# Optimization experiments

Measured on AMD Instinct MI355X. Metric: run time of the kernel, lower is better.

## Reference

```python
import jax, jax.numpy as jnp
import numpy as np

B, S, H, J, LAT, OBS = 256, 128, 1024, 12, 64, 51
NL = 13                  # fk_model link count
PD = (NL + 1) * 3        # pos_dim = 42
FPS = 30.0
ACT_SCALE = 0.25
SMIN, SMAX = 0.05, 0.5
PIN = 2 * J + OBS + LAT  # 139


def setup_inputs() -> dict:
    key = jax.random.key(0)
    ks = jax.random.split(key, 16)
    rn = lambda k, shape, s=0.02: jax.random.normal(k, shape, dtype=jnp.float32) * s
    return dict(
        z=jax.random.normal(ks[0], (B, LAT), jnp.float32),
        obs_seq=jax.random.normal(ks[1], (B, S, OBS), jnp.float32),
        W1=rn(ks[2], (H, PIN)), b1=jnp.zeros((H,), jnp.float32),
        g1=jnp.ones((H,), jnp.float32), be1=jnp.zeros((H,), jnp.float32),
        W2=rn(ks[3], (H, H)), b2=jnp.zeros((H,), jnp.float32),
        g2=jnp.ones((H,), jnp.float32), be2=jnp.zeros((H,), jnp.float32),
        Wa1=rn(ks[4], (H, H)), ba1=jnp.zeros((H,), jnp.float32),
        Wa2=rn(ks[5], (J, H)), ba2=jnp.zeros((J,), jnp.float32),
        Wo=rn(ks[6], (3, H)), bo=jnp.zeros((3,), jnp.float32),
        Wv=rn(ks[7], (PD, H)), bv=jnp.full((PD,), -2.0, jnp.float32),  # torch init: zeros weight, bias=-2 (we keep small random W for non-degenerate grads)
        alpha_logits=jnp.full((J,), float(np.log(0.3)), jnp.float32),
        fk_W=rn(ks[8], (NL * 3, J), 0.1), fk_b=rn(ks[9], (NL * 3,), 0.1),  # linear FK surrogate
        pos_mean=rn(ks[10], (NL + 1, 3), 0.1),
        pos_std=1.0 + jax.random.uniform(ks[11], (NL + 1, 3), jnp.float32),
        joint_lower=jnp.full((J,), -2.0, jnp.float32),
        joint_upper=jnp.full((J,), 2.0, jnp.float32),
        default_dof_pos=rn(ks[12], (J,), 0.3),
    )


def _layernorm(x, g, b):
    m = jnp.mean(x, axis=-1, keepdims=True)
    v = jnp.var(x, axis=-1, keepdims=True)
    return (x - m) * jax.lax.rsqrt(v + 1e-5) * g + b


def reference(z, obs_seq, W1, b1, g1, be1, W2, b2, g2, be2, Wa1, ba1, Wa2, ba2,
              Wo, bo, Wv, bv, alpha_logits, fk_W, fk_b, pos_mean, pos_std,
              joint_lower, joint_upper, default_dof_pos):
    j_range = (joint_upper - joint_lower) / 2.0
    j_mean = (joint_upper + joint_lower) / 2.0
    alpha = jax.nn.sigmoid(alpha_logits)
    Bsz = z.shape[0]

    def step(carry, obs_t):
        pj, pdq = carry                                 # [B,J] each
        jn = (pj - j_mean) / j_range
        x = jnp.concatenate([jn, pdq, obs_t, z], axis=-1)   # [B,PIN]
        h = jax.nn.relu(_layernorm(x @ W1.T + b1, g1, be1))
        h = jax.nn.relu(_layernorm(h @ W2.T + b2, g2, be2))  # [B,H]
        a = jnp.tanh(jax.nn.relu(h @ Wa1.T + ba1) @ Wa2.T + ba2)  # [B,J]
        tgt = a * ACT_SCALE + default_dof_pos
        cj = jnp.clip(pj + alpha * (tgt - pj), joint_lower, joint_upper)
        obj = h @ Wo.T + bo                             # [B,3]
        # torch detaches the carried state (prev_joints/prev_dq)
        cdq = (cj - pj) * FPS
        new_carry = (jax.lax.stop_gradient(cj), jax.lax.stop_gradient(cdq))
        return new_carry, (h, a, cj, obj)

    pj0 = jnp.broadcast_to(default_dof_pos, (Bsz, J))
    pdq0 = jnp.zeros((Bsz, J), z.dtype)
    _, (hs, acts, joints, objs) = jax.lax.scan(step, (pj0, pdq0), jnp.swapaxes(obs_seq, 0, 1))

    features_seq = jnp.swapaxes(hs, 0, 1)    # [B,S,H]
    actions_seq = jnp.swapaxes(acts, 0, 1)   # [B,S,J]
    joint_traj = jnp.swapaxes(joints, 0, 1)  # [B,S,J]
    object_traj = jnp.swapaxes(objs, 0, 1)   # [B,S,3]

    agent_traj = joint_traj @ fk_W.T + fk_b  # [B,S,NL*3] linear FK surrogate
    combined = jnp.concatenate([agent_traj, object_traj], axis=-1)
    combined = combined.reshape(Bsz, S, NL + 1, 3)
    graph_x_mu = ((combined - pos_mean) / pos_std).reshape(Bsz, S, -1)  # [B,S,PD]

    sigma = SMIN + (SMAX - SMIN) * jax.nn.sigmoid(features_seq @ Wv.T + bv)
    log_sigma_pos = jnp.log(sigma)           # [B,S,PD]
    return (graph_x_mu, joint_traj, actions_seq, log_sigma_pos)
```

## Files before the change

### kernel.cpp

```cpp
#include <hip/hip_runtime.h>
#include <math.h>


#define NB 256
#define NS 128
#define NH 1024
#define NJ 12
#define NPIN 139
#define NPD 42
#define WPG 32
#define BROW 32
#define W2S 1032
#define AS 1032
#define XJS 40
#define SLOTSTRIDE 1024

typedef __attribute__((ext_vector_type(8))) short short8;
typedef __attribute__((ext_vector_type(4))) float f32x4;
typedef __attribute__((ext_vector_type(4))) unsigned short u16x4;

struct Params {
  const float* z; const float* obs; const float* W1; const float* b1;
  const float* g1; const float* be1; const float* W2; const float* b2;
  const float* g2; const float* be2; const float* Wa1; const float* ba1;
  const float* Wa2; const float* ba2; const float* Wo; const float* bo;
  const float* Wv; const float* bv; const float* alog; const float* fkW;
  const float* fkb; const float* pmean; const float* pstd; const float* jlo;
  const float* jhi; const float* ddp;
  float* out_gmu; float* out_joint; float* out_act; float* out_ls;
  float* zc; float* pa; float* part2;
  unsigned short* y1b; unsigned short* y2b;
  unsigned short* wa1b; unsigned short* wexb; unsigned short* w1ab;
  unsigned int* gcnt; unsigned int* slots;
};

__device__ __forceinline__ unsigned short f2bf(float x) {
  union { float f; unsigned u; } v; v.f = x;
  unsigned r = v.u + 0x7FFFu + ((v.u >> 16) & 1u);
  return (unsigned short)(r >> 16);
}
__device__ __forceinline__ float bf2f(unsigned short x) {
  union { unsigned u; float f; } v; v.u = ((unsigned)x) << 16;
  return v.f;
}
__device__ __forceinline__ unsigned cvt_pk_bf16(float lo, float hi) {
  unsigned r;
  asm("v_cvt_pk_bf16_f32 %0, %1, %2" : "=v"(r) : "v"(lo), "v"(hi));
  return r;
}
__device__ __forceinline__ void ld16_sc0(const unsigned short* p, short8& d) {
  asm volatile("global_load_dwordx4 %0, %1, off sc0" : "=v"(d) : "v"(p));
}
__device__ __forceinline__ void ldf4_sc0(const float* p, f32x4& d) {
  asm volatile("global_load_dwordx4 %0, %1, off sc0" : "=v"(d) : "v"(p));
}
__device__ __forceinline__ void vwait0() {
  asm volatile("s_waitcnt vmcnt(0)" ::: "memory");
  __builtin_amdgcn_sched_barrier(0);
}

__device__ __forceinline__ f32x4 dot1024(const unsigned short* a, const unsigned short* b) {
  const short8* ap = (const short8*)a;
  const short8* bp = (const short8*)b;
  f32x4 acc0 = {0.f, 0.f, 0.f, 0.f};
  f32x4 acc1 = {0.f, 0.f, 0.f, 0.f};
#pragma unroll 4
  for (int k8 = 0; k8 < 128; k8 += 8) {
    acc0 = __builtin_amdgcn_mfma_f32_16x16x32_bf16(ap[k8], bp[k8], acc0, 0, 0, 0);
    acc1 = __builtin_amdgcn_mfma_f32_16x16x32_bf16(ap[k8 + 4], bp[k8 + 4], acc1, 0, 0, 0);
  }
  return acc0 + acc1;
}

__device__ __forceinline__ void gbar(unsigned int* c, unsigned int target) {
  __threadfence();
  __syncthreads();
  if (threadIdx.x == 0) {
    __hip_atomic_fetch_add(c, 1u, __ATOMIC_RELEASE, __HIP_MEMORY_SCOPE_AGENT);
    unsigned long long t0 = __builtin_amdgcn_s_memrealtime();
    while (__hip_atomic_load(c, __ATOMIC_ACQUIRE, __HIP_MEMORY_SCOPE_AGENT) < target) {
      __builtin_amdgcn_s_sleep(16);
      if (__builtin_amdgcn_s_memrealtime() - t0 > (1ull << 25)) break;
    }
  }
  __syncthreads();
  __threadfence();
}

__device__ __forceinline__ void slot_wait(const unsigned int* sg, unsigned target, int lane) {
  const unsigned int* myslot = sg + (size_t)(lane & 31) * SLOTSTRIDE;
  unsigned long long t0 = __builtin_amdgcn_s_memrealtime();
  for (;;) {
    unsigned v;
    asm volatile("global_load_dword %0, %1, off sc0 sc1\n\t"
                 "s_waitcnt vmcnt(0)"
                 : "=v"(v) : "v"(myslot) : "memory");
    if (__all(v >= target)) break;
    __builtin_amdgcn_s_sleep(1);
    if (__builtin_amdgcn_s_memrealtime() - t0 > (1ull << 23)) break;
  }
}
__device__ __forceinline__ void xbar2(unsigned int* sg, int w, unsigned target,
                                      int wave, int lane) {
  asm volatile("s_waitcnt vmcnt(0)" ::: "memory");
  __syncthreads();
  if (wave == 0) {
    if (lane == 0)
      __hip_atomic_fetch_add(sg + (size_t)w * SLOTSTRIDE, 1u, __ATOMIC_RELAXED,
                             __HIP_MEMORY_SCOPE_AGENT);
    slot_wait(sg, target, lane);
  }
  __syncthreads();
}

__global__ __launch_bounds__(256, 1) void decoder_persistent(Params p) {
  __shared__ unsigned short w2l[BROW * W2S];
  __shared__ unsigned short albuf[BROW * AS];
  __shared__ float g1l[NH], be1l[NH], g2l[NH], be2l[NH];
  __shared__ unsigned short t1l[BROW * 40];
  __shared__ unsigned short wa2l[16 * 40];
  __shared__ unsigned short xjl[BROW * XJS];
  __shared__ float pj_l[BROW * NJ], pdq_l[BROW * NJ];
  __shared__ float alpha_l[NJ], jm_l[NJ], jri_l[NJ], lo_l[NJ], hi_l[NJ], ddp_l[NJ], ba2_l[NJ];
  __shared__ float pm_l[NPD], psi_l[NPD], bv_l[NPD], bo_l[4];

  const int tid = threadIdx.x;
  const int bid = blockIdx.x;
  const int g = bid & 7;
  const int w = bid >> 3;
  const int b0 = g * BROW;
  const int n0 = w * 32;
  const int wave = tid >> 6;
  const int lane = tid & 63;

  unsigned int* sg = p.slots + (size_t)g * WPG * SLOTSTRIDE;
  unsigned short* y1bg = p.y1b + (size_t)g * BROW * NH;
  unsigned short* y2bg = p.y2b + (size_t)g * BROW * NH;
  float* pa_gg = p.pa + (size_t)g * BROW * NJ * 32;
  float* part2g = p.part2 + (size_t)g * BROW * 128;

  if (tid < NJ) {
    alpha_l[tid] = 1.f / (1.f + expf(-p.alog[tid]));
    float lo = p.jlo[tid], hi = p.jhi[tid];
    jm_l[tid] = 0.5f * (hi + lo);
    jri_l[tid] = 2.f / (hi - lo);
    lo_l[tid] = lo; hi_l[tid] = hi;
    ddp_l[tid] = p.ddp[tid]; ba2_l[tid] = p.ba2[tid];
  }
  if (tid < NPD) { pm_l[tid] = p.pmean[tid]; psi_l[tid] = 1.f / p.pstd[tid]; bv_l[tid] = p.bv[tid]; }
  if (tid < 3) bo_l[tid] = p.bo[tid];
  for (int idx = tid; idx < BROW * NJ; idx += 256) { pj_l[idx] = p.ddp[idx % NJ]; pdq_l[idx] = 0.f; }
  for (int idx = tid; idx < NH; idx += 256) {
    g1l[idx] = p.g1[idx]; be1l[idx] = p.be1[idx];
    g2l[idx] = p.g2[idx]; be2l[idx] = p.be2[idx];
  }
  for (int idx = tid; idx < BROW * NH; idx += 256) {
    int r = idx >> 10, k = idx & (NH - 1);
    w2l[r * W2S + k] = f2bf(p.W2[(size_t)(n0 + r) * NH + k]);
  }
  for (int idx = tid; idx < 16 * 32; idx += 256) {
    int rr = idx >> 5, cc = idx & 31;
    wa2l[rr * 40 + cc] = (rr < NJ) ? f2bf(p.Wa2[(size_t)rr * NH + n0 + cc]) : (unsigned short)0;
  }
  __syncthreads();
  for (int idx = tid; idx < BROW * 32; idx += 256) {
    int r = idx >> 5, k = idx & 31;
    float v = 0.f;
    if (k < NJ) v = (pj_l[r * NJ + k] - jm_l[k]) * jri_l[k];
    else if (k < 24) v = pdq_l[r * NJ + (k - 12)];
    xjl[r * XJS + k] = f2bf(v);
  }
  {
    int r = tid >> 3, cq = tid & 7;
    int nb = n0 + cq * 4;
    const float* zr = p.z + (size_t)(b0 + r) * 64;
    const float* w1z = p.W1 + (size_t)nb * NPIN + 75;
    float a0 = p.b1[nb], a1 = p.b1[nb + 1], a2 = p.b1[nb + 2], a3 = p.b1[nb + 3];
    for (int k = 0; k < 64; ++k) {
      float zv = zr[k];
      a0 += zv * w1z[k]; a1 += zv * w1z[NPIN + k];
      a2 += zv * w1z[2 * NPIN + k]; a3 += zv * w1z[3 * NPIN + k];
    }
    f32x4 st = {a0, a1, a2, a3};
    *(f32x4*)(p.zc + (size_t)(b0 + r) * NH + nb) = st;
    const float* w1r = p.W1 + (size_t)nb * NPIN;
    const float* ob = p.obs + (size_t)(b0 + r) * NS * 51;
    for (int o = 0; o < 51; ++o) {
      float ov = ob[o];
      st[0] += ov * w1r[24 + o]; st[1] += ov * w1r[NPIN + 24 + o];
      st[2] += ov * w1r[2 * NPIN + 24 + o]; st[3] += ov * w1r[3 * NPIN + 24 + o];
    }
    u16x4 hv = {f2bf(st[0]), f2bf(st[1]), f2bf(st[2]), f2bf(st[3])};
    *(u16x4*)(y1bg + (size_t)r * NH + nb) = hv;
  }
  for (int idx = tid; idx < 4 * NH; idx += 256) {
    int r = idx >> 10, k = idx & (NH - 1);
    int row = n0 + g * 4 + r;
    p.wa1b[(size_t)row * NH + k] = f2bf(p.Wa1[(size_t)row * NH + k]);
  }
  if (tid < 128) {
    int c2 = tid >> 5, k = tid & 31;
    int col = n0 + g * 4 + c2;
    p.w1ab[(size_t)col * 32 + k] =
        (k < 24) ? f2bf(p.W1[(size_t)col * NPIN + k]) : (unsigned short)0;
  }
  if (bid == 1) {
    for (int idx = tid; idx < 48 * NH; idx += 256) {
      int r = idx >> 10, k = idx & (NH - 1);
      unsigned short v = 0;
      if (r < 3) v = f2bf(p.Wo[(size_t)r * NH + k]);
      else if (r < 45) v = f2bf(p.Wv[(size_t)(r - 3) * NH + k]);
      p.wexb[idx] = v;
    }
  }
  gbar(p.gcnt, 256u);

  auto Ycorr = [&]() {
    const int kq = (lane >> 4) * 8;
    const int r0 = (lane >> 4) * 4;
    short8 a0 = *(const short8*)&xjl[(lane & 15) * XJS + kq];
    short8 a1 = *(const short8*)&xjl[(16 + (lane & 15)) * XJS + kq];
#pragma unroll
    for (int nt = 0; nt < 16; ++nt) {
      int col = (wave * 16 + nt) * 16 + (lane & 15);
      short8 b8 = *(const short8*)(p.w1ab + (size_t)col * 32 + kq);
      f32x4 z4 = {0.f, 0.f, 0.f, 0.f};
      f32x4 d0 = __builtin_amdgcn_mfma_f32_16x16x32_bf16(a0, b8, z4, 0, 0, 0);
      f32x4 d1 = __builtin_amdgcn_mfma_f32_16x16x32_bf16(a1, b8, z4, 0, 0, 0);
#pragma unroll
      for (int i = 0; i < 4; ++i) {
        albuf[(r0 + i) * AS + col] = f2bf(d0[i]);
        albuf[(16 + r0 + i) * AS + col] = f2bf(d1[i]);
      }
    }
  };

  auto Ystage = [&]() {
    const int r = tid >> 3, cq = tid & 7;
    const unsigned short* src = y1bg + (size_t)r * NH + cq * 8;
    unsigned short* dst = &albuf[r * AS + cq * 8];
    short8 vp[16];
#pragma unroll
    for (int i = 0; i < 16; ++i) ld16_sc0(src + (size_t)i * 64, vp[i]);
    vwait0();
    float s = 0.f, q = 0.f;
#pragma unroll
    for (int i = 0; i < 16; ++i) {
      short8 vc = *(const short8*)(dst + i * 64);
      short8 vs;
#pragma unroll
      for (int jj = 0; jj < 8; ++jj) {
        float x = bf2f((unsigned short)vp[i][jj]) + bf2f((unsigned short)vc[jj]);
        s += x; q = fmaf(x, x, q);
        vs[jj] = (short)f2bf(x);
      }
      vp[i] = vs;
    }
#pragma unroll
    for (int off = 4; off; off >>= 1) {
      s += __shfl_down(s, off, 8);
      q += __shfl_down(q, off, 8);
    }
    s = __shfl(s, 0, 8); q = __shfl(q, 0, 8);
    float m = s * (1.f / 1024.f);
    float rs = rsqrtf(q * (1.f / 1024.f) - m * m + 1e-5f);
    float nmrs = -m * rs;
#pragma unroll
    for (int i = 0; i < 16; ++i) {
      int c = cq * 8 + i * 64;
      f32x4 ga = *(const f32x4*)(g1l + c);
      f32x4 gb = *(const f32x4*)(g1l + c + 4);
      f32x4 ba = *(const f32x4*)(be1l + c);
      f32x4 bb = *(const f32x4*)(be1l + c + 4);
      float xn[8];
#pragma unroll
      for (int jj = 0; jj < 8; ++jj) {
        float x = bf2f((unsigned short)vp[i][jj]);
        float tn = fmaf(x, rs, nmrs);
        float gg = (jj < 4) ? ga[jj] : gb[jj - 4];
        float bv2 = (jj < 4) ? ba[jj] : bb[jj - 4];
        xn[jj] = fmaxf(fmaf(tn, gg, bv2), 0.f);
      }
      uint4 pk = {cvt_pk_bf16(xn[0], xn[1]), cvt_pk_bf16(xn[2], xn[3]),
                  cvt_pk_bf16(xn[4], xn[5]), cvt_pk_bf16(xn[6], xn[7])};
      *(uint4*)(dst + i * 64) = pk;
    }
  };

  auto Yphase = [&]() {
    Ycorr();
    __syncthreads();
    Ystage();
    __syncthreads();
    int rt = wave >> 1, ct = wave & 1;
    int kq = (lane >> 4) * 8;
    const unsigned short* a = &albuf[(rt * 16 + (lane & 15)) * AS + kq];
    const unsigned short* b = &w2l[(ct * 16 + (lane & 15)) * W2S + kq];
    f32x4 acc = dot1024(a, b);
    int col = n0 + ct * 16 + (lane & 15);
    float b2v = p.b2[col];
    float sv[4], qv[4];
#pragma unroll
    for (int i = 0; i < 4; ++i) {
      int row = rt * 16 + (lane >> 4) * 4 + i;
      float val = acc[i] + b2v;
      y2bg[(size_t)row * NH + col] = f2bf(val);
      sv[i] = val; qv[i] = val * val;
    }
#pragma unroll
    for (int mask = 1; mask < 16; mask <<= 1) {
#pragma unroll
      for (int i = 0; i < 4; ++i) {
        sv[i] += __shfl_xor(sv[i], mask, 64);
        qv[i] += __shfl_xor(qv[i], mask, 64);
      }
    }
    if ((lane & 15) == 0) {
      int rbase = rt * 16 + (lane >> 4) * 4;
#pragma unroll
      for (int i = 0; i < 4; ++i) {
        float* pw = part2g + (size_t)(rbase + i) * 128 + (w * 2 + ct) * 2;
        pw[0] = sv[i]; pw[1] = qv[i];
      }
    }
  };

  auto Zstage = [&]() {
    const int r = tid >> 3, cq = tid & 7;
    const unsigned short* src = y2bg + (size_t)r * NH + cq * 8;
    unsigned short* dst = &albuf[r * AS + cq * 8];
    short8 v[16];
#pragma unroll
    for (int i = 0; i < 16; ++i) ld16_sc0(src + (size_t)i * 64, v[i]);
    const float* pp = part2g + (size_t)r * 128 + cq * 16;
    f32x4 p0, p1, p2, p3;
    ldf4_sc0(pp, p0); ldf4_sc0(pp + 4, p1);
    ldf4_sc0(pp + 8, p2); ldf4_sc0(pp + 12, p3);
    vwait0();
    float s = p0[0] + p0[2] + p1[0] + p1[2] + p2[0] + p2[2] + p3[0] + p3[2];
    float q = p0[1] + p0[3] + p1[1] + p1[3] + p2[1] + p2[3] + p3[1] + p3[3];
#pragma unroll
    for (int off = 4; off; off >>= 1) {
      s += __shfl_down(s, off, 8);
      q += __shfl_down(q, off, 8);
    }
    s = __shfl(s, 0, 8); q = __shfl(q, 0, 8);
    float m = s * (1.f / 1024.f);
    float rs = rsqrtf(q * (1.f / 1024.f) - m * m + 1e-5f);
    float nmrs = -m * rs;
#pragma unroll
    for (int i = 0; i < 16; ++i) {
      int c = cq * 8 + i * 64;
      f32x4 ga = *(const f32x4*)(g2l + c);
      f32x4 gb = *(const f32x4*)(g2l + c + 4);
      f32x4 ba = *(const f32x4*)(be2l + c);
      f32x4 bb = *(const f32x4*)(be2l + c + 4);
      float xn[8];
#pragma unroll
      for (int jj = 0; jj < 8; ++jj) {
        float x = bf2f((unsigned short)v[i][jj]);
        float tn = fmaf(x, rs, nmrs);
        float gg = (jj < 4) ? ga[jj] : gb[jj - 4];
        float bv2 = (jj < 4) ? ba[jj] : bb[jj - 4];
        xn[jj] = fmaxf(fmaf(tn, gg, bv2), 0.f);
      }
      uint4 pk = {cvt_pk_bf16(xn[0], xn[1]), cvt_pk_bf16(xn[2], xn[3]),
                  cvt_pk_bf16(xn[4], xn[5]), cvt_pk_bf16(xn[6], xn[7])};
      *(uint4*)(dst + i * 64) = pk;
    }
  };

  auto Zphase = [&](int t) {
    Zstage();
    __syncthreads();
    int rt = wave >> 1, ct = wave & 1;
    int kq = (lane >> 4) * 8;
    {
      const unsigned short* a = &albuf[(rt * 16 + (lane & 15)) * AS + kq];
      const unsigned short* b = p.wa1b + (size_t)(n0 + ct * 16 + (lane & 15)) * NH + kq;
      f32x4 acc = dot1024(a, b);
      int lcol = ct * 16 + (lane & 15);
      float bav = p.ba1[n0 + lcol];
#pragma unroll
      for (int i = 0; i < 4; ++i) {
        int row = rt * 16 + (lane >> 4) * 4 + i;
        t1l[row * 40 + lcol] = f2bf(fmaxf(acc[i] + bav, 0.f));
      }
    }
    __syncthreads();
    if (wave < 2) {
      int k0 = (lane >> 4) * 8;
      short8 a8 = *(const short8*)&t1l[(wave * 16 + (lane & 15)) * 40 + k0];
      short8 b8 = *(const short8*)&wa2l[(lane & 15) * 40 + k0];
      f32x4 z4 = {0.f, 0.f, 0.f, 0.f};
      f32x4 d = __builtin_amdgcn_mfma_f32_16x16x32_bf16(a8, b8, z4, 0, 0, 0);
      int j = lane & 15;
      if (j < NJ) {
#pragma unroll
        for (int i = 0; i < 4; ++i) {
          int row = wave * 16 + (lane >> 4) * 4 + i;
          pa_gg[((size_t)row * NJ + j) * 32 + w] = d[i];
        }
      }
    }
    if (w >= 26 && wave == 3) {
      int e = w - 26, cte = e >> 1, rte = e & 1;
      const unsigned short* a = &albuf[(rte * 16 + (lane & 15)) * AS + kq];
      const unsigned short* b = p.wexb + (size_t)(cte * 16 + (lane & 15)) * NH + kq;
      f32x4 acc = dot1024(a, b);
      int ec = cte * 16 + (lane & 15);
#pragma unroll
      for (int i = 0; i < 4; ++i) {
        int row = rte * 16 + (lane >> 4) * 4 + i;
        int bb = b0 + row;
        if (ec < 3) {
          float val = acc[i] + bo_l[ec];
          p.out_gmu[((size_t)bb * NS + t) * NPD + 39 + ec] = (val - pm_l[39 + ec]) * psi_l[39 + ec];
        } else if (ec < 45) {
          int sv2 = ec - 3;
          float val = acc[i] + bv_l[sv2];
          float sig = 0.05f + 0.45f / (1.f + expf(-val));
          p.out_ls[((size_t)bb * NS + t) * NPD + sv2] = logf(sig);
        }
      }
    }
    if (t + 1 < NS) {
      int r = tid >> 3, cq = tid & 7;
      int nb = n0 + cq * 4;
      f32x4 acc = *(const f32x4*)(p.zc + (size_t)(b0 + r) * NH + nb);
      const float* w1r = p.W1 + (size_t)nb * NPIN;
      const float* ob = p.obs + ((size_t)(b0 + r) * NS + (t + 1)) * 51;
      for (int o = 0; o < 51; ++o) {
        float ov = ob[o];
        acc[0] += ov * w1r[24 + o]; acc[1] += ov * w1r[NPIN + 24 + o];
        acc[2] += ov * w1r[2 * NPIN + 24 + o]; acc[3] += ov * w1r[3 * NPIN + 24 + o];
      }
      u16x4 hv = {f2bf(acc[0]), f2bf(acc[1]), f2bf(acc[2]), f2bf(acc[3])};
      *(u16x4*)(y1bg + (size_t)r * NH + nb) = hv;
    }
  };

  auto Xmid = [&](int tp) {
    for (int e = tid; e < BROW * NJ; e += 256) {
      const float* pp = pa_gg + (size_t)e * 32;
      f32x4 u[8];
#pragma unroll
      for (int c2 = 0; c2 < 8; ++c2) ldf4_sc0(pp + c2 * 4, u[c2]);
      vwait0();
      f32x4 ss = ((u[0] + u[1]) + (u[2] + u[3])) + ((u[4] + u[5]) + (u[6] + u[7]));
      float sum = ss[0] + ss[1] + ss[2] + ss[3];
      int r = e / NJ, j = e - r * NJ;
      float av = tanhf(sum + ba2_l[j]);
      float pj = pj_l[e];
      float tgt = av * 0.25f + ddp_l[j];
      float cj = pj + alpha_l[j] * (tgt - pj);
      cj = fminf(fmaxf(cj, lo_l[j]), hi_l[j]);
      pdq_l[e] = (cj - pj) * 30.f;
      pj_l[e] = cj;
      if (w == 0) {
        size_t o = ((size_t)(b0 + r) * NS + tp) * NJ + j;
        p.out_joint[o] = cj;
        p.out_act[o] = av;
      }
    }
    __syncthreads();
    if (w == 0) {
      for (int idx = tid; idx < BROW * 39; idx += 256) {
        int r = idx / 39, m = idx - r * 39;
        float s = p.fkb[m];
        const float* fw = p.fkW + m * NJ;
#pragma unroll
        for (int j = 0; j < NJ; ++j) s += pj_l[r * NJ + j] * fw[j];
        p.out_gmu[((size_t)(b0 + r) * NS + tp) * NPD + m] = (s - pm_l[m]) * psi_l[m];
      }
    }
    for (int idx = tid; idx < BROW * 32; idx += 256) {
      int r = idx >> 5, k = idx & 31;
      float v = 0.f;
      if (k < NJ) v = (pj_l[r * NJ + k] - jm_l[k]) * jri_l[k];
      else if (k < 24) v = pdq_l[r * NJ + (k - 12)];
      xjl[r * XJS + k] = f2bf(v);
    }
    __syncthreads();
  };

  unsigned nbar = 0;
  for (int t = 0; t < NS; ++t) {
    Yphase();
    xbar2(sg, w, ++nbar, wave, lane);
    Zphase(t);
    xbar2(sg, w, ++nbar, wave, lane);
    Xmid(t);
  }
}

extern "C" void kernel_launch(void* const* d_in, const int* in_sizes, int n_in,
                              void* d_out, int out_size, void* d_ws, size_t ws_size,
                              hipStream_t stream) {
  (void)in_sizes; (void)n_in; (void)out_size; (void)ws_size;
  char* ws = (char*)d_ws;
  Params p;
  p.z = (const float*)d_in[0];   p.obs = (const float*)d_in[1];
  p.W1 = (const float*)d_in[2];  p.b1 = (const float*)d_in[3];
  p.g1 = (const float*)d_in[4];  p.be1 = (const float*)d_in[5];
  p.W2 = (const float*)d_in[6];  p.b2 = (const float*)d_in[7];
  p.g2 = (const float*)d_in[8];  p.be2 = (const float*)d_in[9];
  p.Wa1 = (const float*)d_in[10]; p.ba1 = (const float*)d_in[11];
  p.Wa2 = (const float*)d_in[12]; p.ba2 = (const float*)d_in[13];
  p.Wo = (const float*)d_in[14]; p.bo = (const float*)d_in[15];
  p.Wv = (const float*)d_in[16]; p.bv = (const float*)d_in[17];
  p.alog = (const float*)d_in[18];
  p.fkW = (const float*)d_in[19]; p.fkb = (const float*)d_in[20];
  p.pmean = (const float*)d_in[21]; p.pstd = (const float*)d_in[22];
  p.jlo = (const float*)d_in[23]; p.jhi = (const float*)d_in[24];
  p.ddp = (const float*)d_in[25];

  float* out = (float*)d_out;
  p.out_gmu = out;
  p.out_joint = out + (size_t)256 * 128 * 42;
  p.out_act = p.out_joint + (size_t)256 * 128 * 12;
  p.out_ls = p.out_act + (size_t)256 * 128 * 12;

  p.gcnt = (unsigned int*)(ws + 0);
  p.slots = (unsigned int*)(ws + 4096);
  size_t off = 4096 + (size_t)8 * WPG * SLOTSTRIDE * 4;
  p.zc = (float*)(ws + off);                 off += (size_t)NB * NH * 4;
  p.y1b = (unsigned short*)(ws + off);       off += (size_t)NB * NH * 2;
  p.y2b = (unsigned short*)(ws + off);       off += (size_t)NB * NH * 2;
  p.pa = (float*)(ws + off);                 off += (size_t)8 * 32 * 12 * 32 * 4;
  p.part2 = (float*)(ws + off);              off += (size_t)8 * 32 * 128 * 4;
  p.wa1b = (unsigned short*)(ws + off);      off += (size_t)NH * NH * 2;
  p.wexb = (unsigned short*)(ws + off);      off += (size_t)48 * NH * 2;
  p.w1ab = (unsigned short*)(ws + off);      off += (size_t)NH * 32 * 2;

  hipMemsetAsync(d_ws, 0, 4096 + (size_t)8 * WPG * SLOTSTRIDE * 4, stream);
  decoder_persistent<<<dim3(256), dim3(256), 0, stream>>>(p);
}
```

Measured before the change: 3.718 ms.

## Double-buffer y1 and compute next-step obs projection inside the barrier wait

Splits the cross-block barrier after the Y phase into an arrive and a wait. Between them, each block computes the next timestep's obs/z input projection into a double-buffered y1 buffer, so this work overlaps the barrier latency. Previously it ran at the end of the Z phase on the critical path. The cost is twice the y1 workspace and an extra buffer-index selection per step.

```diff
diff --git a/kernel.cpp b/kernel.cpp
--- a/kernel.cpp
+++ b/kernel.cpp
@@ -134,7 +134,8 @@
   const int lane = tid & 63;
 
   unsigned int* sg = p.slots + (size_t)g * WPG * SLOTSTRIDE;
-  unsigned short* y1bg = p.y1b + (size_t)g * BROW * NH;
+  unsigned short* y1b0 = p.y1b + (size_t)g * BROW * NH;
+  unsigned short* y1b1 = p.y1b + (size_t)NB * NH + (size_t)g * BROW * NH;
   unsigned short* y2bg = p.y2b + (size_t)g * BROW * NH;
   float* pa_gg = p.pa + (size_t)g * BROW * NJ * 32;
   float* part2g = p.part2 + (size_t)g * BROW * 128;
@@ -191,7 +192,7 @@
       st[2] += ov * w1r[2 * NPIN + 24 + o]; st[3] += ov * w1r[3 * NPIN + 24 + o];
     }
     u16x4 hv = {f2bf(st[0]), f2bf(st[1]), f2bf(st[2]), f2bf(st[3])};
-    *(u16x4*)(y1bg + (size_t)r * NH + nb) = hv;
+    *(u16x4*)(y1b0 + (size_t)r * NH + nb) = hv;
   }
   for (int idx = tid; idx < 4 * NH; idx += 256) {
     int r = idx >> 10, k = idx & (NH - 1);
@@ -235,7 +236,7 @@
     }
   };
 
-  auto Ystage = [&]() {
+  auto Ystage = [&](const unsigned short* y1bg) {
     const int r = tid >> 3, cq = tid & 7;
     const unsigned short* src = y1bg + (size_t)r * NH + cq * 8;
     unsigned short* dst = &albuf[r * AS + cq * 8];
@@ -287,10 +288,10 @@
     }
   };
 
-  auto Yphase = [&]() {
+  auto Yphase = [&](const unsigned short* y1bg) {
     Ycorr();
     __syncthreads();
-    Ystage();
+    Ystage(y1bg);
     __syncthreads();
     int rt = wave >> 1, ct = wave & 1;
     int kq = (lane >> 4) * 8;
@@ -323,6 +324,21 @@
         pw[0] = sv[i]; pw[1] = qv[i];
       }
     }
+  };
+
+  auto P1p = [&](int t, unsigned short* dst) {
+    int r = tid >> 3, cq = tid & 7;
+    int nb = n0 + cq * 4;
+    f32x4 acc = *(const f32x4*)(p.zc + (size_t)(b0 + r) * NH + nb);
+    const float* w1r = p.W1 + (size_t)nb * NPIN;
+    const float* ob = p.obs + ((size_t)(b0 + r) * NS + t) * 51;
+    for (int o = 0; o < 51; ++o) {
+      float ov = ob[o];
+      acc[0] += ov * w1r[24 + o]; acc[1] += ov * w1r[NPIN + 24 + o];
+      acc[2] += ov * w1r[2 * NPIN + 24 + o]; acc[3] += ov * w1r[3 * NPIN + 24 + o];
+    }
+    u16x4 hv = {f2bf(acc[0]), f2bf(acc[1]), f2bf(acc[2]), f2bf(acc[3])};
+    *(u16x4*)(dst + (size_t)r * NH + nb) = hv;
   };
 
   auto Zstage = [&]() {
@@ -423,20 +439,6 @@
           p.out_ls[((size_t)bb * NS + t) * NPD + sv2] = logf(sig);
         }
       }
-    }
-    if (t + 1 < NS) {
-      int r = tid >> 3, cq = tid & 7;
-      int nb = n0 + cq * 4;
-      f32x4 acc = *(const f32x4*)(p.zc + (size_t)(b0 + r) * NH + nb);
-      const float* w1r = p.W1 + (size_t)nb * NPIN;
-      const float* ob = p.obs + ((size_t)(b0 + r) * NS + (t + 1)) * 51;
-      for (int o = 0; o < 51; ++o) {
-        float ov = ob[o];
-        acc[0] += ov * w1r[24 + o]; acc[1] += ov * w1r[NPIN + 24 + o];
-        acc[2] += ov * w1r[2 * NPIN + 24 + o]; acc[3] += ov * w1r[3 * NPIN + 24 + o];
-      }
-      u16x4 hv = {f2bf(acc[0]), f2bf(acc[1]), f2bf(acc[2]), f2bf(acc[3])};
-      *(u16x4*)(y1bg + (size_t)r * NH + nb) = hv;
     }
   };
 
@@ -486,8 +488,18 @@
 
   unsigned nbar = 0;
   for (int t = 0; t < NS; ++t) {
-    Yphase();
-    xbar2(sg, w, ++nbar, wave, lane);
+    Yphase((t & 1) ? y1b1 : y1b0);
+    {
+      unsigned tb = ++nbar;
+      asm volatile("s_waitcnt vmcnt(0)" ::: "memory");
+      __syncthreads();
+      if (tid == 0)
+        __hip_atomic_fetch_add(sg + (size_t)w * SLOTSTRIDE, 1u, __ATOMIC_RELAXED,
+                               __HIP_MEMORY_SCOPE_AGENT);
+      if (t + 1 < NS) P1p(t + 1, ((t + 1) & 1) ? y1b1 : y1b0);
+      if (wave == 0) slot_wait(sg, tb, lane);
+      __syncthreads();
+    }
     Zphase(t);
     xbar2(sg, w, ++nbar, wave, lane);
     Xmid(t);
@@ -525,7 +537,7 @@
   p.slots = (unsigned int*)(ws + 4096);
   size_t off = 4096 + (size_t)8 * WPG * SLOTSTRIDE * 4;
   p.zc = (float*)(ws + off);                 off += (size_t)NB * NH * 4;
-  p.y1b = (unsigned short*)(ws + off);       off += (size_t)NB * NH * 2;
+  p.y1b = (unsigned short*)(ws + off);       off += (size_t)2 * NB * NH * 2;
   p.y2b = (unsigned short*)(ws + off);       off += (size_t)NB * NH * 2;
   p.pa = (float*)(ws + off);                 off += (size_t)8 * 32 * 12 * 32 * 4;
   p.part2 = (float*)(ws + off);              off += (size_t)8 * 32 * 128 * 4;
```

New measurement: 3.669 ms. Within noise of the previous version (-1.3%).
